# Kernel optimization log

Measured on AMD Instinct MI355X. Metric: run time of the kernel, lower is better.

## Reference

```python
import jax, jax.numpy as jnp
import numpy as np

N = 65536   # base nodes
M = 65536   # union local nodes
E = 1048576 # base edges
EL = 1048576 # local edges
K = 131072  # membership entries
F = 128     # in_channels
H = 128     # hidden_dim
L = 2       # num_layers
OUT = 2
ALPHA = 0.9


def setup_inputs() -> dict:
    key = jax.random.key(0)
    ks = jax.random.split(key, 16)
    s = 1.0 / np.sqrt(H)
    return {
        "x": jax.random.normal(ks[0], (N, F), jnp.float32),
        "edge_index": jax.random.randint(ks[1], (2, E), 0, N, jnp.int64 if jax.config.jax_enable_x64 else jnp.int32),
        "edge_weight": jax.random.uniform(ks[2], (E,), jnp.float32),
        "local_x0": jax.random.normal(ks[3], (M, F), jnp.float32),
        "copy2orig": jax.random.randint(ks[4], (M,), 0, N),
        "local_adj_index": jax.random.randint(ks[5], (2, EL), 0, M),
        "local_adj_value": jax.random.uniform(ks[6], (EL,), jnp.float32),
        "memb_idx": jax.random.randint(ks[7], (K,), 0, M),
        "memb_gid": jax.random.randint(ks[8], (K,), 0, 64),
        "B": 64,
        "Wb_in": jax.random.normal(ks[9], (F, H), jnp.float32) * s,
        "bb_in": jnp.zeros((H,), jnp.float32),
        "Wl_in": jax.random.normal(ks[10], (F, H), jnp.float32) * s,
        "bl_in": jnp.zeros((H,), jnp.float32),
        "W_base": jax.random.normal(ks[11], (L, H, H), jnp.float32) * s,
        "b_base": jnp.zeros((L, H), jnp.float32),
        "W_local": jax.random.normal(ks[12], (L, H, H), jnp.float32) * s,
        "b_local": jnp.zeros((L, H), jnp.float32),
        "Wp": jax.random.normal(ks[13], (H, OUT), jnp.float32) * s,
        "bp": jnp.zeros((OUT,), jnp.float32),
    }


def reference(x, edge_index, edge_weight, local_x0, copy2orig, local_adj_index,
              local_adj_value, memb_idx, memb_gid, B, Wb_in, bb_in, Wl_in, bl_in,
              W_base, b_base, W_local, b_local, Wp, bp):
    n = x.shape[0]
    m = local_x0.shape[0]
    # input projections (dropout is identity in eval mode)
    base_x = jax.nn.relu(x @ Wb_in + bb_in)
    local_x = jax.nn.relu(local_x0 @ Wl_in + bl_in)
    src, dst = edge_index[0], edge_index[1]
    lsrc, ldst = local_adj_index[0], local_adj_index[1]
    for l in range(W_base.shape[0]):
        # base graph propagation: normalized-adjacency spmm then linear+relu
        base_agg = jax.ops.segment_sum(base_x[src] * edge_weight[:, None], dst, num_segments=n)
        base_x = jax.nn.relu(base_agg @ W_base[l] + b_base[l])
        # local union-graph propagation + alpha-mix with base features via copy2orig
        local_agg = jax.ops.segment_sum(local_x[lsrc] * local_adj_value[:, None], ldst, num_segments=m)
        mix = ALPHA * local_agg + (1.0 - ALPHA) * base_x[copy2orig]
        local_x = jax.nn.relu(mix @ W_local[l] + b_local[l])
    # scatter-mean pooling by membership (fused sum + count)
    sub = jax.ops.segment_sum(local_x[memb_idx], memb_gid, num_segments=B)
    cnt = jax.ops.segment_sum(jnp.ones((memb_gid.shape[0], 1), local_x.dtype), memb_gid, num_segments=B)
    sub = sub / jnp.maximum(cnt, 1.0)
    return sub @ Wp + bp
```

## Files before the change

### kernel.cpp

```cpp
#include <hip/hip_runtime.h>

typedef __attribute__((ext_vector_type(8))) short bfrag;
typedef __attribute__((ext_vector_type(4))) float ffrag;

__device__ __forceinline__ ushort f2bf(float f) {
    union { float f; unsigned u; } v{f};
    unsigned r = v.u + 0x7fff + ((v.u >> 16) & 1);
    return (ushort)(r >> 16);
}
__device__ __forceinline__ float bf2f(ushort u) {
    union { unsigned u; float f; } v{(unsigned)u << 16};
    return v.f;
}
__device__ __forceinline__ float bflo(unsigned u) {
    union { unsigned u; float f; } v{u << 16};
    return v.f;
}
__device__ __forceinline__ float bfhi(unsigned u) {
    union { unsigned u; float f; } v{u & 0xffff0000u};
    return v.f;
}

#define WDEC (1.f / 65535.f)


__global__ __launch_bounds__(256) void wprep_zero(const float* __restrict__ Wb_in, const float* __restrict__ Wl_in,
                                                  const float* __restrict__ W_base, const float* __restrict__ W_local,
                                                  ushort* __restrict__ out,
                                                  int* __restrict__ z_a, int* __restrict__ z_b,
                                                  int* __restrict__ z_c, int* __restrict__ z_d) {
    const int bid = blockIdx.x;
    const int t = threadIdx.x;
    if (bid < 384) {
        int idx = bid * 256 + t;
        int mat = idx >> 14;
        int i = idx & 16383;
        int nn = i >> 7, kk = i & 127;
        const float* src;
        switch (mat) {
            case 0: src = Wb_in; break;
            case 1: src = Wl_in; break;
            case 2: src = W_base; break;
            case 3: src = W_base + 16384; break;
            case 4: src = W_local; break;
            default: src = W_local + 16384; break;
        }
        out[(size_t)mat * 16384 + i] = f2bf(src[kk * 128 + nn]);
    } else {
        int i = (bid - 384) * 256 + t;
        if (i < 512) { z_a[i] = 0; z_b[i] = 0; }
        if (i < 64) z_c[i] = 0;
        z_d[i] = 0;
    }
}


#define NB 512
#define BSH 7
#define CH2 2048

__global__ __launch_bounds__(256) void bhist2(const int* __restrict__ b_dst, const int* __restrict__ l_dst,
                                              int* __restrict__ b_cnt, int* __restrict__ l_cnt) {
    __shared__ int h[NB];
    const int t = threadIdx.x;
    h[t] = 0;
    h[t + 256] = 0;
    __syncthreads();
    const int g = blockIdx.x >> 8;
    const int* dst = g ? l_dst : b_dst;
    int* cnt = g ? l_cnt : b_cnt;
    const int base = (blockIdx.x & 255) * 4096;
#pragma unroll
    for (int u = 0; u < 16; ++u)
        atomicAdd(&h[((unsigned)dst[base + u * 256 + t]) >> BSH], 1);
    __syncthreads();
    atomicAdd(&cnt[t], h[t]);
    atomicAdd(&cnt[t + 256], h[t + 256]);
}

__global__ __launch_bounds__(512) void bscan2(const int* __restrict__ b_cnt, int* __restrict__ b_sta, int* __restrict__ b_cur,
                                              const int* __restrict__ l_cnt, int* __restrict__ l_sta, int* __restrict__ l_cur) {
    __shared__ int s[NB];
    const int t = threadIdx.x;
    const int* cnt = blockIdx.x ? l_cnt : b_cnt;
    int* sta = blockIdx.x ? l_sta : b_sta;
    int* cur = blockIdx.x ? l_cur : b_cur;
    int c = cnt[t];
    s[t] = c;
    __syncthreads();
    for (int o = 1; o < NB; o <<= 1) {
        int add = (t >= o) ? s[t - o] : 0;
        __syncthreads();
        s[t] += add;
        __syncthreads();
    }
    sta[t] = s[t] - c;
    cur[t] = s[t] - c;
    if (t == NB - 1) sta[NB] = s[t];
}

__global__ __launch_bounds__(1024) void bucket1b(const int* __restrict__ b_src, const int* __restrict__ b_dst,
                                                 const float* __restrict__ b_w, int* __restrict__ b_cur,
                                                 int2* __restrict__ b_staged,
                                                 const int* __restrict__ l_src, const int* __restrict__ l_dst,
                                                 const float* __restrict__ l_w, int* __restrict__ l_cur,
                                                 int2* __restrict__ l_staged) {
    __shared__ int cnt_s[NB], base_l[NB], base_g[NB], curs[NB];
    __shared__ int2 stage[CH2];
    __shared__ ushort bb[CH2];
    const int t = threadIdx.x;
    const int g = blockIdx.x >> 9;
    const int* src = g ? l_src : b_src;
    const int* dst = g ? l_dst : b_dst;
    const float* w = g ? l_w : b_w;
    int* bcursor = g ? l_cur : b_cur;
    int2* staged = g ? l_staged : b_staged;
    const int base = (blockIdx.x & 511) * CH2;
    if (t < NB) cnt_s[t] = 0;
    __syncthreads();
#pragma unroll
    for (int u = 0; u < CH2 / 1024; ++u) {
        int b = ((unsigned)dst[base + u * 1024 + t]) >> BSH;
        atomicAdd(&cnt_s[b], 1);
    }
    __syncthreads();
    int v = 0;
    if (t < NB) { v = cnt_s[t]; base_l[t] = v; }
    __syncthreads();
    for (int o = 1; o < NB; o <<= 1) {
        int add = 0;
        if (t < NB && t >= o) add = base_l[t - o];
        __syncthreads();
        if (t < NB) base_l[t] += add;
        __syncthreads();
    }
    if (t < NB) {
        int excl = base_l[t] - v;
        base_l[t] = excl;
        curs[t] = excl;
        base_g[t] = atomicAdd(&bcursor[t], v);
    }
    __syncthreads();
#pragma unroll
    for (int u = 0; u < CH2 / 1024; ++u) {
        int e = base + u * 1024 + t;
        int d = dst[e];
        int b = ((unsigned)d) >> BSH;
        int p = atomicAdd(&curs[b], 1);
        stage[p] = make_int2((src[e] & 0xffff) | ((d & 127) << 16), __float_as_int(w[e]));
        bb[p] = (ushort)b;
    }
    __syncthreads();
    for (int i = t; i < CH2; i += 1024) {
        int b = bb[i];
        staged[base_g[b] + (i - base_l[b])] = stage[i];
    }
}

__global__ __launch_bounds__(1024) void bucket2b(const int* __restrict__ b_sta, const int2* __restrict__ b_staged,
                                                 int* __restrict__ b_start, int* __restrict__ b_edges,
                                                 const int* __restrict__ l_sta, const int2* __restrict__ l_staged,
                                                 int* __restrict__ l_start, int* __restrict__ l_edges) {
    __shared__ int cnt[128], excl[128], curs[128];
    const int t = threadIdx.x;
    const int g = blockIdx.x >> 9;
    const int b = blockIdx.x & 511;
    const int* bsta = g ? l_sta : b_sta;
    const int2* staged = g ? l_staged : b_staged;
    int* start = g ? l_start : b_start;
    int* edges = g ? l_edges : b_edges;
    if (t < 128) cnt[t] = 0;
    __syncthreads();
    const int s0 = bsta[b];
    const int s1 = bsta[b + 1];
    for (int i = s0 + t; i < s1; i += 1024) {
        int dl = (staged[i].x >> 16) & 127;
        atomicAdd(&cnt[dl], 1);
    }
    __syncthreads();
    int v = 0;
    if (t < 128) { v = cnt[t]; excl[t] = v; }
    __syncthreads();
    for (int o = 1; o < 128; o <<= 1) {
        int add = 0;
        if (t < 128 && t >= o) add = excl[t - o];
        __syncthreads();
        if (t < 128) excl[t] += add;
        __syncthreads();
    }
    if (t < 128) {
        int e = excl[t] - v;
        curs[t] = e;
        start[b * 128 + t] = s0 + e;
        if (b == 511 && t == 127) start[65536] = s1;
    }
    __syncthreads();
    for (int i = s0 + t; i < s1; i += 1024) {
        int2 se = staged[i];
        int dl = (se.x >> 16) & 127;
        int p = s0 + atomicAdd(&curs[dl], 1);
        float wv = __int_as_float(se.y);
        unsigned wq = (unsigned)(wv * 65535.f + 0.5f);
        edges[p] = (int)(((unsigned)se.x & 0xffffu) | (wq << 16));
    }
}

#define ASTRIDE 136


__global__ __launch_bounds__(256) void gemm_in2(const float* __restrict__ Ab, const float* __restrict__ Al,
                                                const ushort* __restrict__ Wt,
                                                const float* __restrict__ biasb, const float* __restrict__ biasl,
                                                ushort* __restrict__ Yb, ushort* __restrict__ Yl) {
    __shared__ ushort As[64 * ASTRIDE];
    __shared__ ushort Bs[128 * ASTRIDE];
    const int tid = threadIdx.x;
    const int g = blockIdx.x >> 10;
    const float* A = g ? Al : Ab;
    const ushort* W = Wt + (size_t)g * 16384;
    const float* bias = g ? biasl : biasb;
    ushort* Y = g ? Yl : Yb;
    const int r0 = (blockIdx.x & 1023) * 64;

#pragma unroll
    for (int p = 0; p < 8; ++p) {
        int c = p * 256 + tid;
        int row = c >> 5, o4 = (c & 31) * 4;
        float4 v = *(const float4*)(A + (size_t)(r0 + row) * 128 + o4);
        ushort4 u;
        u.x = f2bf(v.x); u.y = f2bf(v.y); u.z = f2bf(v.z); u.w = f2bf(v.w);
        *(ushort4*)&As[row * ASTRIDE + o4] = u;
    }
#pragma unroll
    for (int p = 0; p < 8; ++p) {
        int c = p * 256 + tid;
        int n = c >> 4, o8 = (c & 15) * 8;
        *(uint4*)&Bs[n * ASTRIDE + o8] = *(const uint4*)(W + n * 128 + o8);
    }
    __syncthreads();

    const int lane = tid & 63;
    const int w = tid >> 6;
    const int wm = (w & 1) * 32;
    const int wn = (w >> 1) * 64;
    const int q = lane >> 4;
    const int l16 = lane & 15;

    ffrag acc[2][4];
#pragma unroll
    for (int mt = 0; mt < 2; ++mt)
#pragma unroll
        for (int nt = 0; nt < 4; ++nt) acc[mt][nt] = (ffrag){0.f, 0.f, 0.f, 0.f};

#pragma unroll
    for (int kc = 0; kc < 4; ++kc) {
        bfrag a[2], b[4];
#pragma unroll
        for (int mt = 0; mt < 2; ++mt)
            a[mt] = *(const bfrag*)&As[(wm + mt * 16 + l16) * ASTRIDE + kc * 32 + q * 8];
#pragma unroll
        for (int nt = 0; nt < 4; ++nt)
            b[nt] = *(const bfrag*)&Bs[(wn + nt * 16 + l16) * ASTRIDE + kc * 32 + q * 8];
#pragma unroll
        for (int mt = 0; mt < 2; ++mt)
#pragma unroll
            for (int nt = 0; nt < 4; ++nt)
                acc[mt][nt] = __builtin_amdgcn_mfma_f32_16x16x32_bf16(a[mt], b[nt], acc[mt][nt], 0, 0, 0);
    }

    float bias_v[4];
#pragma unroll
    for (int nt = 0; nt < 4; ++nt) bias_v[nt] = bias[wn + nt * 16 + l16];
#pragma unroll
    for (int mt = 0; mt < 2; ++mt)
#pragma unroll
        for (int nt = 0; nt < 4; ++nt)
#pragma unroll
            for (int r = 0; r < 4; ++r) {
                int row = r0 + wm + mt * 16 + q * 4 + r;
                int col = wn + nt * 16 + l16;
                float v = fmaxf(acc[mt][nt][r] + bias_v[nt], 0.f);
                Y[(size_t)row * 128 + col] = f2bf(v);
            }
}


template <bool MIX>
__global__ __launch_bounds__(256) void gemm_layer(const ushort* __restrict__ A, const ushort* __restrict__ A2,
                                                  const int* __restrict__ ridx,
                                                  const ushort* __restrict__ Wt, const float* __restrict__ bias,
                                                  ushort* __restrict__ Y) {
    __shared__ ushort As[64 * ASTRIDE];
    __shared__ ushort Bs[128 * ASTRIDE];
    const int tid = threadIdx.x;
    const int r0 = blockIdx.x * 64;

#pragma unroll
    for (int p = 0; p < 4; ++p) {
        int c = p * 256 + tid;
        int row = c >> 4, o8 = (c & 15) * 8;
        uint4 v = *(const uint4*)(A + (size_t)(r0 + row) * 128 + o8);
        if (MIX) {
            int rr = ridx[r0 + row];
            uint4 v2 = *(const uint4*)(A2 + (size_t)rr * 128 + o8);
            uint4 o;
            float x0, x1;
            x0 = 0.9f * bflo(v.x) + 0.1f * bflo(v2.x);
            x1 = 0.9f * bfhi(v.x) + 0.1f * bfhi(v2.x);
            o.x = (unsigned)f2bf(x0) | ((unsigned)f2bf(x1) << 16);
            x0 = 0.9f * bflo(v.y) + 0.1f * bflo(v2.y);
            x1 = 0.9f * bfhi(v.y) + 0.1f * bfhi(v2.y);
            o.y = (unsigned)f2bf(x0) | ((unsigned)f2bf(x1) << 16);
            x0 = 0.9f * bflo(v.z) + 0.1f * bflo(v2.z);
            x1 = 0.9f * bfhi(v.z) + 0.1f * bfhi(v2.z);
            o.z = (unsigned)f2bf(x0) | ((unsigned)f2bf(x1) << 16);
            x0 = 0.9f * bflo(v.w) + 0.1f * bflo(v2.w);
            x1 = 0.9f * bfhi(v.w) + 0.1f * bfhi(v2.w);
            o.w = (unsigned)f2bf(x0) | ((unsigned)f2bf(x1) << 16);
            v = o;
        }
        *(uint4*)&As[row * ASTRIDE + o8] = v;
    }
#pragma unroll
    for (int p = 0; p < 8; ++p) {
        int c = p * 256 + tid;
        int n = c >> 4, o8 = (c & 15) * 8;
        *(uint4*)&Bs[n * ASTRIDE + o8] = *(const uint4*)(Wt + n * 128 + o8);
    }
    __syncthreads();

    const int lane = tid & 63;
    const int w = tid >> 6;
    const int wm = (w & 1) * 32;
    const int wn = (w >> 1) * 64;
    const int q = lane >> 4;
    const int l16 = lane & 15;

    ffrag acc[2][4];
#pragma unroll
    for (int mt = 0; mt < 2; ++mt)
#pragma unroll
        for (int nt = 0; nt < 4; ++nt) acc[mt][nt] = (ffrag){0.f, 0.f, 0.f, 0.f};

#pragma unroll
    for (int kc = 0; kc < 4; ++kc) {
        bfrag a[2], b[4];
#pragma unroll
        for (int mt = 0; mt < 2; ++mt)
            a[mt] = *(const bfrag*)&As[(wm + mt * 16 + l16) * ASTRIDE + kc * 32 + q * 8];
#pragma unroll
        for (int nt = 0; nt < 4; ++nt)
            b[nt] = *(const bfrag*)&Bs[(wn + nt * 16 + l16) * ASTRIDE + kc * 32 + q * 8];
#pragma unroll
        for (int mt = 0; mt < 2; ++mt)
#pragma unroll
            for (int nt = 0; nt < 4; ++nt)
                acc[mt][nt] = __builtin_amdgcn_mfma_f32_16x16x32_bf16(a[mt], b[nt], acc[mt][nt], 0, 0, 0);
    }

    float bias_v[4];
#pragma unroll
    for (int nt = 0; nt < 4; ++nt) bias_v[nt] = bias[wn + nt * 16 + l16];
#pragma unroll
    for (int mt = 0; mt < 2; ++mt)
#pragma unroll
        for (int nt = 0; nt < 4; ++nt)
#pragma unroll
            for (int r = 0; r < 4; ++r) {
                int row = r0 + wm + mt * 16 + q * 4 + r;
                int col = wn + nt * 16 + l16;
                float v = fmaxf(acc[mt][nt][r] + bias_v[nt], 0.f);
                Y[(size_t)row * 128 + col] = f2bf(v);
            }
}


__global__ __launch_bounds__(256) void spmm2(const int* __restrict__ bs_start, const int* __restrict__ bs_edges,
                                             const ushort* __restrict__ Xb, ushort* __restrict__ Yb,
                                             const int* __restrict__ ls_start, const int* __restrict__ ls_edges,
                                             const ushort* __restrict__ Xl, ushort* __restrict__ Yl) {
    const int g = blockIdx.x & 1;
    const int* start = g ? ls_start : bs_start;
    const int* edges = g ? ls_edges : bs_edges;
    const ushort* X = g ? Xl : Xb;
    ushort* Y = g ? Yl : Yb;
    int node = (((blockIdx.x >> 1) * 256) + threadIdx.x) >> 5;
    int lane = threadIdx.x & 31;
    int s0 = start[node];
    int s1 = start[node + 1];
    const int f = lane * 4;
    float a0 = 0.f, a1 = 0.f, a2 = 0.f, a3 = 0.f;
    int e = s0;
    for (; e < s1 && (e & 3); ++e) {
        unsigned pe = (unsigned)edges[e];
        float w = (float)(pe >> 16) * WDEC;
        ushort4 v = *(const ushort4*)(X + ((size_t)(pe & 0xffffu) << 7) + f);
        a0 += w * bf2f(v.x); a1 += w * bf2f(v.y); a2 += w * bf2f(v.z); a3 += w * bf2f(v.w);
    }
    for (; e + 8 <= s1; e += 8) {
        int4 pA = *(const int4*)(edges + e);
        int4 pB = *(const int4*)(edges + e + 4);
        ushort4 v0 = *(const ushort4*)(X + ((size_t)((unsigned)pA.x & 0xffffu) << 7) + f);
        ushort4 v1 = *(const ushort4*)(X + ((size_t)((unsigned)pA.y & 0xffffu) << 7) + f);
        ushort4 v2 = *(const ushort4*)(X + ((size_t)((unsigned)pA.z & 0xffffu) << 7) + f);
        ushort4 v3 = *(const ushort4*)(X + ((size_t)((unsigned)pA.w & 0xffffu) << 7) + f);
        ushort4 v4 = *(const ushort4*)(X + ((size_t)((unsigned)pB.x & 0xffffu) << 7) + f);
        ushort4 v5 = *(const ushort4*)(X + ((size_t)((unsigned)pB.y & 0xffffu) << 7) + f);
        ushort4 v6 = *(const ushort4*)(X + ((size_t)((unsigned)pB.z & 0xffffu) << 7) + f);
        ushort4 v7 = *(const ushort4*)(X + ((size_t)((unsigned)pB.w & 0xffffu) << 7) + f);
        float w0 = (float)((unsigned)pA.x >> 16) * WDEC;
        float w1 = (float)((unsigned)pA.y >> 16) * WDEC;
        float w2 = (float)((unsigned)pA.z >> 16) * WDEC;
        float w3 = (float)((unsigned)pA.w >> 16) * WDEC;
        float w4 = (float)((unsigned)pB.x >> 16) * WDEC;
        float w5 = (float)((unsigned)pB.y >> 16) * WDEC;
        float w6 = (float)((unsigned)pB.z >> 16) * WDEC;
        float w7 = (float)((unsigned)pB.w >> 16) * WDEC;
        a0 += w0 * bf2f(v0.x) + w1 * bf2f(v1.x) + w2 * bf2f(v2.x) + w3 * bf2f(v3.x)
            + w4 * bf2f(v4.x) + w5 * bf2f(v5.x) + w6 * bf2f(v6.x) + w7 * bf2f(v7.x);
        a1 += w0 * bf2f(v0.y) + w1 * bf2f(v1.y) + w2 * bf2f(v2.y) + w3 * bf2f(v3.y)
            + w4 * bf2f(v4.y) + w5 * bf2f(v5.y) + w6 * bf2f(v6.y) + w7 * bf2f(v7.y);
        a2 += w0 * bf2f(v0.z) + w1 * bf2f(v1.z) + w2 * bf2f(v2.z) + w3 * bf2f(v3.z)
            + w4 * bf2f(v4.z) + w5 * bf2f(v5.z) + w6 * bf2f(v6.z) + w7 * bf2f(v7.z);
        a3 += w0 * bf2f(v0.w) + w1 * bf2f(v1.w) + w2 * bf2f(v2.w) + w3 * bf2f(v3.w)
            + w4 * bf2f(v4.w) + w5 * bf2f(v5.w) + w6 * bf2f(v6.w) + w7 * bf2f(v7.w);
    }
    for (; e + 4 <= s1; e += 4) {
        int4 pA = *(const int4*)(edges + e);
        ushort4 v0 = *(const ushort4*)(X + ((size_t)((unsigned)pA.x & 0xffffu) << 7) + f);
        ushort4 v1 = *(const ushort4*)(X + ((size_t)((unsigned)pA.y & 0xffffu) << 7) + f);
        ushort4 v2 = *(const ushort4*)(X + ((size_t)((unsigned)pA.z & 0xffffu) << 7) + f);
        ushort4 v3 = *(const ushort4*)(X + ((size_t)((unsigned)pA.w & 0xffffu) << 7) + f);
        float w0 = (float)((unsigned)pA.x >> 16) * WDEC;
        float w1 = (float)((unsigned)pA.y >> 16) * WDEC;
        float w2 = (float)((unsigned)pA.z >> 16) * WDEC;
        float w3 = (float)((unsigned)pA.w >> 16) * WDEC;
        a0 += w0 * bf2f(v0.x) + w1 * bf2f(v1.x) + w2 * bf2f(v2.x) + w3 * bf2f(v3.x);
        a1 += w0 * bf2f(v0.y) + w1 * bf2f(v1.y) + w2 * bf2f(v2.y) + w3 * bf2f(v3.y);
        a2 += w0 * bf2f(v0.z) + w1 * bf2f(v1.z) + w2 * bf2f(v2.z) + w3 * bf2f(v3.z);
        a3 += w0 * bf2f(v0.w) + w1 * bf2f(v1.w) + w2 * bf2f(v2.w) + w3 * bf2f(v3.w);
    }
    for (; e < s1; ++e) {
        unsigned pe = (unsigned)edges[e];
        float w = (float)(pe >> 16) * WDEC;
        ushort4 v = *(const ushort4*)(X + ((size_t)(pe & 0xffffu) << 7) + f);
        a0 += w * bf2f(v.x); a1 += w * bf2f(v.y); a2 += w * bf2f(v.z); a3 += w * bf2f(v.w);
    }
    ushort4 o;
    o.x = f2bf(a0);
    o.y = f2bf(a1);
    o.z = f2bf(a2);
    o.w = f2bf(a3);
    *(ushort4*)(Y + (size_t)node * 128 + f) = o;
}


__global__ __launch_bounds__(256) void pool_hist(const int* __restrict__ memb_gid, int* __restrict__ gcount) {
    __shared__ int h[64];
    int t = threadIdx.x;
    if (t < 64) h[t] = 0;
    __syncthreads();
    int base = blockIdx.x * 1024;
#pragma unroll
    for (int u = 0; u < 4; ++u) atomicAdd(&h[memb_gid[base + u * 256 + t]], 1);
    __syncthreads();
    if (t < 64) atomicAdd(&gcount[t], h[t]);
}

__global__ __launch_bounds__(64) void pool_scan(const int* __restrict__ gcount, int* __restrict__ gstart,
                                                int* __restrict__ cursor) {
    __shared__ int s[64];
    int t = threadIdx.x;
    int c = gcount[t];
    s[t] = c;
    __syncthreads();
    int acc = 0;
    for (int j = 0; j < 64; ++j)
        if (j < t) acc += s[j];
    gstart[t] = acc;
    cursor[t] = acc;
    if (t == 63) gstart[64] = acc + c;
}

__global__ __launch_bounds__(256) void pool_scatter(const int* __restrict__ memb_idx,
                                                    const int* __restrict__ memb_gid,
                                                    int* __restrict__ cursor, int* __restrict__ sorted_idx) {
    __shared__ int lhist[64];
    __shared__ int lbase[64];
    __shared__ int loff[1024];
    int t = threadIdx.x;
    if (t < 64) lhist[t] = 0;
    __syncthreads();
    int base = blockIdx.x * 1024;
    int g[4], ix[4];
#pragma unroll
    for (int u = 0; u < 4; ++u) {
        int e = base + u * 256 + t;
        g[u] = memb_gid[e];
        ix[u] = memb_idx[e];
        loff[u * 256 + t] = atomicAdd(&lhist[g[u]], 1);
    }
    __syncthreads();
    if (t < 64) lbase[t] = atomicAdd(&cursor[t], lhist[t]);
    __syncthreads();
#pragma unroll
    for (int u = 0; u < 4; ++u) {
        int pos = lbase[g[u]] + loff[u * 256 + t];
        sorted_idx[pos] = ix[u];
    }
}

__global__ __launch_bounds__(256) void pool_accum(const int* __restrict__ gstart, const int* __restrict__ sorted_idx,
                                                  const ushort* __restrict__ X, float* __restrict__ gsum) {
    const int g = blockIdx.x >> 5;
    const int sgm = blockIdx.x & 31;
    const int gs = gstart[g];
    const int cnt = gstart[g + 1] - gs;
    const int e_begin = gs + ((cnt * sgm) >> 5);
    const int e_end = gs + ((cnt * (sgm + 1)) >> 5);
    const int t = threadIdx.x;
    const int fp = t & 63;
    const int sub = t >> 6;
    float ax = 0.f, ay = 0.f;
#pragma unroll 4
    for (int e = e_begin + sub; e < e_end; e += 4) {
        int idx = sorted_idx[e];
        ushort2 u = *(const ushort2*)(X + (size_t)idx * 128 + fp * 2);
        ax += bf2f(u.x);
        ay += bf2f(u.y);
    }
    __shared__ float sx[256], sy[256];
    sx[t] = ax;
    sy[t] = ay;
    __syncthreads();
    if (t < 64) {
        atomicAdd(&gsum[g * 128 + fp * 2 + 0], sx[t] + sx[t + 64] + sx[t + 128] + sx[t + 192]);
        atomicAdd(&gsum[g * 128 + fp * 2 + 1], sy[t] + sy[t + 64] + sy[t + 128] + sy[t + 192]);
    }
}


__global__ __launch_bounds__(128) void final_kernel(const float* __restrict__ gsum, const int* __restrict__ gcnt,
                                                    const float* __restrict__ Wp, const float* __restrict__ bp,
                                                    float* __restrict__ out) {
    int t = threadIdx.x;
    int g = t >> 1;
    int o = t & 1;
    float inv = 1.f / fmaxf((float)gcnt[g], 1.f);
    float acc = bp[o];
    for (int f = 0; f < 128; ++f) acc += gsum[g * 128 + f] * inv * Wp[f * 2 + o];
    out[g * 2 + o] = acc;
}


extern "C" void kernel_launch(void* const* d_in, const int* in_sizes, int n_in,
                              void* d_out, int out_size, void* d_ws, size_t ws_size,
                              hipStream_t stream) {
    const float* x              = (const float*)d_in[0];
    const int*   edge_index     = (const int*)d_in[1];
    const float* edge_weight    = (const float*)d_in[2];
    const float* local_x0       = (const float*)d_in[3];
    const int*   copy2orig      = (const int*)d_in[4];
    const int*   local_adj_idx  = (const int*)d_in[5];
    const float* local_adj_val  = (const float*)d_in[6];
    const int*   memb_idx       = (const int*)d_in[7];
    const int*   memb_gid       = (const int*)d_in[8];
    const float* Wb_in          = (const float*)d_in[10];
    const float* bb_in          = (const float*)d_in[11];
    const float* Wl_in          = (const float*)d_in[12];
    const float* bl_in          = (const float*)d_in[13];
    const float* W_base         = (const float*)d_in[14];
    const float* b_base         = (const float*)d_in[15];
    const float* W_local        = (const float*)d_in[16];
    const float* b_local        = (const float*)d_in[17];
    const float* Wp             = (const float*)d_in[18];
    const float* bp             = (const float*)d_in[19];
    float* out = (float*)d_out;

    constexpr int N = 65536, M = 65536, E = 1048576, EL = 1048576, K = 131072, H = 128;

    char* wsb = (char*)d_ws;
    size_t off = 0;
    auto alloc = [&](size_t bytes) -> char* {
        char* p = wsb + off;
        off += (bytes + 255) & ~(size_t)255;
        return p;
    };
    int*    bs_start = (int*)alloc((size_t)(N + 1) * 4);
    int*    bs_edges = (int*)alloc((size_t)E * 4);
    int2*   bs_stage = (int2*)alloc((size_t)E * 8);
    int*    bs_bcnt  = (int*)alloc(NB * 4);
    int*    bs_bsta  = (int*)alloc((NB + 1) * 4);
    int*    bs_bcur  = (int*)alloc(NB * 4);
    int*    ls_start = (int*)alloc((size_t)(M + 1) * 4);
    int*    ls_edges = (int*)alloc((size_t)EL * 4);
    int2*   ls_stage = (int2*)alloc((size_t)EL * 8);
    int*    ls_bcnt  = (int*)alloc(NB * 4);
    int*    ls_bsta  = (int*)alloc((NB + 1) * 4);
    int*    ls_bcur  = (int*)alloc(NB * 4);
    ushort* bufA     = (ushort*)alloc((size_t)N * H * 2);
    ushort* bufB     = (ushort*)alloc((size_t)M * H * 2);
    ushort* bufC     = (ushort*)alloc((size_t)N * H * 2);
    ushort* bufD     = (ushort*)alloc((size_t)M * H * 2);
    ushort* wt       = (ushort*)alloc((size_t)6 * 16384 * 2);
    int*    p_gcnt   = (int*)alloc(64 * 4);
    int*    p_gstart = (int*)alloc(65 * 4);
    int*    p_cursor = (int*)alloc(64 * 4);
    int*    p_sorted = (int*)alloc((size_t)K * 4);
    float*  pool_sum = (float*)alloc(64 * 128 * 4);

    const int* b_src = edge_index;
    const int* b_dst = edge_index + E;
    const int* l_src = local_adj_idx;
    const int* l_dst = local_adj_idx + EL;

    wprep_zero<<<416, 256, 0, stream>>>(Wb_in, Wl_in, W_base, W_local, wt,
                                        bs_bcnt, ls_bcnt, p_gcnt, (int*)pool_sum);

    bhist2<<<512, 256, 0, stream>>>(b_dst, l_dst, bs_bcnt, ls_bcnt);
    bscan2<<<2, 512, 0, stream>>>(bs_bcnt, bs_bsta, bs_bcur, ls_bcnt, ls_bsta, ls_bcur);
    bucket1b<<<1024, 1024, 0, stream>>>(b_src, b_dst, edge_weight, bs_bcur, bs_stage,
                                        l_src, l_dst, local_adj_val, ls_bcur, ls_stage);
    bucket2b<<<1024, 1024, 0, stream>>>(bs_bsta, bs_stage, bs_start, bs_edges,
                                        ls_bsta, ls_stage, ls_start, ls_edges);

    pool_hist<<<K / 1024, 256, 0, stream>>>(memb_gid, p_gcnt);
    pool_scan<<<1, 64, 0, stream>>>(p_gcnt, p_gstart, p_cursor);
    pool_scatter<<<K / 1024, 256, 0, stream>>>(memb_idx, memb_gid, p_cursor, p_sorted);

    gemm_in2<<<2048, 256, 0, stream>>>(x, local_x0, wt, bb_in, bl_in, bufA, bufB);

    for (int l = 0; l < 2; ++l) {
        spmm2<<<16384, 256, 0, stream>>>(bs_start, bs_edges, bufA, bufC,
                                         ls_start, ls_edges, bufB, bufD);
        gemm_layer<false><<<N / 64, 256, 0, stream>>>(bufC, nullptr, nullptr,
                                                      wt + (size_t)(2 + l) * 16384, b_base + (size_t)l * H, bufA);
        gemm_layer<true><<<M / 64, 256, 0, stream>>>(bufD, bufA, copy2orig,
                                                     wt + (size_t)(4 + l) * 16384, b_local + (size_t)l * H, bufB);
    }

    pool_accum<<<64 * 32, 256, 0, stream>>>(p_gstart, p_sorted, bufB, pool_sum);
    final_kernel<<<1, 128, 0, stream>>>(pool_sum, p_gcnt, Wp, bp, out);
}
```

Before: 424.6 us.

## Build CSR with direct per-node atomics and split SpMM feature halves

Replaces the two-level bucket sort (bucket histogram, staged bucket scatter, per-bucket local sort) with a direct CSR build: per-node global atomic histogram, a three-pass prefix scan, and atomic-cursor scatter of packed edges. This removes the staging buffer and one full pass over the edges, at the cost of heavy global atomic contention and non-deterministic edge order within each row. The SpMM also splits each node's 128 features across two blocks, each lane gathering 2 bf16 values instead of 4. That doubles the grid for more parallelism but rereads the edge lists twice and narrows the gather loads.

```diff
diff --git a/kernel.cpp b/kernel.cpp
--- a/kernel.cpp
+++ b/kernel.cpp
@@ -27,8 +27,8 @@
 __global__ __launch_bounds__(256) void wprep_zero(const float* __restrict__ Wb_in, const float* __restrict__ Wl_in,
                                                   const float* __restrict__ W_base, const float* __restrict__ W_local,
                                                   ushort* __restrict__ out,
-                                                  int* __restrict__ z_a, int* __restrict__ z_b,
-                                                  int* __restrict__ z_c, int* __restrict__ z_d) {
+                                                  int* __restrict__ b_cnt, int* __restrict__ l_cnt,
+                                                  int* __restrict__ gcnt, int* __restrict__ psum) {
     const int bid = blockIdx.x;
     const int t = threadIdx.x;
     if (bid < 384) {
@@ -48,160 +48,104 @@
         out[(size_t)mat * 16384 + i] = f2bf(src[kk * 128 + nn]);
     } else {
         int i = (bid - 384) * 256 + t;
-        if (i < 512) { z_a[i] = 0; z_b[i] = 0; }
-        if (i < 64) z_c[i] = 0;
-        z_d[i] = 0;
-    }
-}
-
-
-#define NB 512
-#define BSH 7
-#define CH2 2048
-
-__global__ __launch_bounds__(256) void bhist2(const int* __restrict__ b_dst, const int* __restrict__ l_dst,
-                                              int* __restrict__ b_cnt, int* __restrict__ l_cnt) {
-    __shared__ int h[NB];
-    const int t = threadIdx.x;
-    h[t] = 0;
-    h[t + 256] = 0;
-    __syncthreads();
-    const int g = blockIdx.x >> 8;
+        if (i < 65536) b_cnt[i] = 0;
+        else if (i < 131072) l_cnt[i - 65536] = 0;
+        else if (i < 131136) gcnt[i - 131072] = 0;
+        else if (i < 139328) psum[i - 131136] = 0;
+    }
+}
+
+
+__global__ __launch_bounds__(256) void csr_hist(const int* __restrict__ b_dst, const int* __restrict__ l_dst,
+                                                int* __restrict__ b_cnt, int* __restrict__ l_cnt) {
+    const int g = blockIdx.x >> 10;
     const int* dst = g ? l_dst : b_dst;
     int* cnt = g ? l_cnt : b_cnt;
-    const int base = (blockIdx.x & 255) * 4096;
-#pragma unroll
-    for (int u = 0; u < 16; ++u)
-        atomicAdd(&h[((unsigned)dst[base + u * 256 + t]) >> BSH], 1);
-    __syncthreads();
-    atomicAdd(&cnt[t], h[t]);
-    atomicAdd(&cnt[t + 256], h[t + 256]);
-}
-
-__global__ __launch_bounds__(512) void bscan2(const int* __restrict__ b_cnt, int* __restrict__ b_sta, int* __restrict__ b_cur,
-                                              const int* __restrict__ l_cnt, int* __restrict__ l_sta, int* __restrict__ l_cur) {
-    __shared__ int s[NB];
+    const int base = (blockIdx.x & 1023) * 1024 + threadIdx.x;
+#pragma unroll
+    for (int u = 0; u < 4; ++u)
+        atomicAdd(&cnt[dst[base + u * 256]], 1);
+}
+
+__global__ __launch_bounds__(256) void csr_scan1(const int* __restrict__ b_cnt, const int* __restrict__ l_cnt,
+                                                 int* __restrict__ b_start, int* __restrict__ l_start,
+                                                 int* __restrict__ bsum) {
+    __shared__ int sh[256];
     const int t = threadIdx.x;
-    const int* cnt = blockIdx.x ? l_cnt : b_cnt;
-    int* sta = blockIdx.x ? l_sta : b_sta;
-    int* cur = blockIdx.x ? l_cur : b_cur;
-    int c = cnt[t];
-    s[t] = c;
-    __syncthreads();
-    for (int o = 1; o < NB; o <<= 1) {
-        int add = (t >= o) ? s[t - o] : 0;
+    const int g = blockIdx.x >> 6;
+    const int blk = blockIdx.x & 63;
+    const int* cnt = g ? l_cnt : b_cnt;
+    int* out = g ? l_start : b_start;
+    int4 v = ((const int4*)cnt)[blk * 256 + t];
+    int s = v.x + v.y + v.z + v.w;
+    sh[t] = s;
+    __syncthreads();
+    for (int o = 1; o < 256; o <<= 1) {
+        int add = (t >= o) ? sh[t - o] : 0;
         __syncthreads();
-        s[t] += add;
+        sh[t] += add;
         __syncthreads();
     }
-    sta[t] = s[t] - c;
-    cur[t] = s[t] - c;
-    if (t == NB - 1) sta[NB] = s[t];
-}
-
-__global__ __launch_bounds__(1024) void bucket1b(const int* __restrict__ b_src, const int* __restrict__ b_dst,
-                                                 const float* __restrict__ b_w, int* __restrict__ b_cur,
-                                                 int2* __restrict__ b_staged,
-                                                 const int* __restrict__ l_src, const int* __restrict__ l_dst,
-                                                 const float* __restrict__ l_w, int* __restrict__ l_cur,
-                                                 int2* __restrict__ l_staged) {
-    __shared__ int cnt_s[NB], base_l[NB], base_g[NB], curs[NB];
-    __shared__ int2 stage[CH2];
-    __shared__ ushort bb[CH2];
+    int excl = sh[t] - s;
+    int4 o4;
+    o4.x = excl;
+    o4.y = excl + v.x;
+    o4.z = excl + v.x + v.y;
+    o4.w = excl + v.x + v.y + v.z;
+    ((int4*)out)[blk * 256 + t] = o4;
+    if (t == 255) bsum[blockIdx.x] = sh[255];
+}
+
+__global__ __launch_bounds__(128) void csr_scan2(const int* __restrict__ bsum, int* __restrict__ bbase,
+                                                 int* __restrict__ b_start, int* __restrict__ l_start) {
+    __shared__ int s[128];
     const int t = threadIdx.x;
-    const int g = blockIdx.x >> 9;
+    s[t] = bsum[t];
+    __syncthreads();
+    const int sb = t & 64;
+    int acc = 0;
+    for (int j = sb; j < t; ++j) acc += s[j];
+    bbase[t] = acc;
+    if (t == 63) b_start[65536] = acc + s[63];
+    if (t == 127) l_start[65536] = acc + s[127];
+}
+
+__global__ __launch_bounds__(256) void csr_scan3(const int* __restrict__ bbase,
+                                                 int* __restrict__ b_start, int* __restrict__ b_cur,
+                                                 int* __restrict__ l_start, int* __restrict__ l_cur) {
+    const int t = threadIdx.x;
+    const int g = blockIdx.x >> 6;
+    const int blk = blockIdx.x & 63;
+    const int off = bbase[blockIdx.x];
+    int* out = g ? l_start : b_start;
+    int* cur = g ? l_cur : b_cur;
+    int4 v = ((const int4*)out)[blk * 256 + t];
+    v.x += off; v.y += off; v.z += off; v.w += off;
+    ((int4*)out)[blk * 256 + t] = v;
+    ((int4*)cur)[blk * 256 + t] = v;
+}
+
+__global__ __launch_bounds__(256) void csr_scatter(const int* __restrict__ b_src, const int* __restrict__ b_dst,
+                                                   const float* __restrict__ b_w, int* __restrict__ b_cur,
+                                                   int* __restrict__ b_edges,
+                                                   const int* __restrict__ l_src, const int* __restrict__ l_dst,
+                                                   const float* __restrict__ l_w, int* __restrict__ l_cur,
+                                                   int* __restrict__ l_edges) {
+    const int g = blockIdx.x >> 10;
     const int* src = g ? l_src : b_src;
     const int* dst = g ? l_dst : b_dst;
     const float* w = g ? l_w : b_w;
-    int* bcursor = g ? l_cur : b_cur;
-    int2* staged = g ? l_staged : b_staged;
-    const int base = (blockIdx.x & 511) * CH2;
-    if (t < NB) cnt_s[t] = 0;
-    __syncthreads();
-#pragma unroll
-    for (int u = 0; u < CH2 / 1024; ++u) {
-        int b = ((unsigned)dst[base + u * 1024 + t]) >> BSH;
-        atomicAdd(&cnt_s[b], 1);
-    }
-    __syncthreads();
-    int v = 0;
-    if (t < NB) { v = cnt_s[t]; base_l[t] = v; }
-    __syncthreads();
-    for (int o = 1; o < NB; o <<= 1) {
-        int add = 0;
-        if (t < NB && t >= o) add = base_l[t - o];
-        __syncthreads();
-        if (t < NB) base_l[t] += add;
-        __syncthreads();
-    }
-    if (t < NB) {
-        int excl = base_l[t] - v;
-        base_l[t] = excl;
-        curs[t] = excl;
-        base_g[t] = atomicAdd(&bcursor[t], v);
-    }
-    __syncthreads();
-#pragma unroll
-    for (int u = 0; u < CH2 / 1024; ++u) {
-        int e = base + u * 1024 + t;
+    int* cur = g ? l_cur : b_cur;
+    int* edges = g ? l_edges : b_edges;
+    const int base = (blockIdx.x & 1023) * 1024 + threadIdx.x;
+#pragma unroll
+    for (int u = 0; u < 4; ++u) {
+        int e = base + u * 256;
         int d = dst[e];
-        int b = ((unsigned)d) >> BSH;
-        int p = atomicAdd(&curs[b], 1);
-        stage[p] = make_int2((src[e] & 0xffff) | ((d & 127) << 16), __float_as_int(w[e]));
-        bb[p] = (ushort)b;
-    }
-    __syncthreads();
-    for (int i = t; i < CH2; i += 1024) {
-        int b = bb[i];
-        staged[base_g[b] + (i - base_l[b])] = stage[i];
-    }
-}
-
-__global__ __launch_bounds__(1024) void bucket2b(const int* __restrict__ b_sta, const int2* __restrict__ b_staged,
-                                                 int* __restrict__ b_start, int* __restrict__ b_edges,
-                                                 const int* __restrict__ l_sta, const int2* __restrict__ l_staged,
-                                                 int* __restrict__ l_start, int* __restrict__ l_edges) {
-    __shared__ int cnt[128], excl[128], curs[128];
-    const int t = threadIdx.x;
-    const int g = blockIdx.x >> 9;
-    const int b = blockIdx.x & 511;
-    const int* bsta = g ? l_sta : b_sta;
-    const int2* staged = g ? l_staged : b_staged;
-    int* start = g ? l_start : b_start;
-    int* edges = g ? l_edges : b_edges;
-    if (t < 128) cnt[t] = 0;
-    __syncthreads();
-    const int s0 = bsta[b];
-    const int s1 = bsta[b + 1];
-    for (int i = s0 + t; i < s1; i += 1024) {
-        int dl = (staged[i].x >> 16) & 127;
-        atomicAdd(&cnt[dl], 1);
-    }
-    __syncthreads();
-    int v = 0;
-    if (t < 128) { v = cnt[t]; excl[t] = v; }
-    __syncthreads();
-    for (int o = 1; o < 128; o <<= 1) {
-        int add = 0;
-        if (t < 128 && t >= o) add = excl[t - o];
-        __syncthreads();
-        if (t < 128) excl[t] += add;
-        __syncthreads();
-    }
-    if (t < 128) {
-        int e = excl[t] - v;
-        curs[t] = e;
-        start[b * 128 + t] = s0 + e;
-        if (b == 511 && t == 127) start[65536] = s1;
-    }
-    __syncthreads();
-    for (int i = s0 + t; i < s1; i += 1024) {
-        int2 se = staged[i];
-        int dl = (se.x >> 16) & 127;
-        int p = s0 + atomicAdd(&curs[dl], 1);
-        float wv = __int_as_float(se.y);
-        unsigned wq = (unsigned)(wv * 65535.f + 0.5f);
-        edges[p] = (int)(((unsigned)se.x & 0xffffu) | (wq << 16));
+        unsigned wq = (unsigned)(w[e] * 65535.f + 0.5f);
+        int packed = (int)(((unsigned)src[e] & 0xffffu) | (wq << 16));
+        int pos = atomicAdd(&cur[d], 1);
+        edges[pos] = packed;
     }
 }
 
@@ -380,34 +324,36 @@
                                              const int* __restrict__ ls_start, const int* __restrict__ ls_edges,
                                              const ushort* __restrict__ Xl, ushort* __restrict__ Yl) {
     const int g = blockIdx.x & 1;
+    const int h = (blockIdx.x >> 1) & 1;
     const int* start = g ? ls_start : bs_start;
     const int* edges = g ? ls_edges : bs_edges;
     const ushort* X = g ? Xl : Xb;
     ushort* Y = g ? Yl : Yb;
-    int node = (((blockIdx.x >> 1) * 256) + threadIdx.x) >> 5;
-    int lane = threadIdx.x & 31;
-    int s0 = start[node];
-    int s1 = start[node + 1];
-    const int f = lane * 4;
-    float a0 = 0.f, a1 = 0.f, a2 = 0.f, a3 = 0.f;
+    const int node = ((blockIdx.x >> 2) * 256 + threadIdx.x) >> 5;
+    const int lane = threadIdx.x & 31;
+    const int fo = h * 64 + lane * 2;
+    const int s0 = start[node];
+    const int s1 = start[node + 1];
+    float a0 = 0.f, a1 = 0.f;
     int e = s0;
     for (; e < s1 && (e & 3); ++e) {
         unsigned pe = (unsigned)edges[e];
         float w = (float)(pe >> 16) * WDEC;
-        ushort4 v = *(const ushort4*)(X + ((size_t)(pe & 0xffffu) << 7) + f);
-        a0 += w * bf2f(v.x); a1 += w * bf2f(v.y); a2 += w * bf2f(v.z); a3 += w * bf2f(v.w);
+        ushort2 v = *(const ushort2*)(X + ((size_t)(pe & 0xffffu) << 7) + fo);
+        a0 += w * bf2f(v.x);
+        a1 += w * bf2f(v.y);
     }
     for (; e + 8 <= s1; e += 8) {
         int4 pA = *(const int4*)(edges + e);
         int4 pB = *(const int4*)(edges + e + 4);
-        ushort4 v0 = *(const ushort4*)(X + ((size_t)((unsigned)pA.x & 0xffffu) << 7) + f);
-        ushort4 v1 = *(const ushort4*)(X + ((size_t)((unsigned)pA.y & 0xffffu) << 7) + f);
-        ushort4 v2 = *(const ushort4*)(X + ((size_t)((unsigned)pA.z & 0xffffu) << 7) + f);
-        ushort4 v3 = *(const ushort4*)(X + ((size_t)((unsigned)pA.w & 0xffffu) << 7) + f);
-        ushort4 v4 = *(const ushort4*)(X + ((size_t)((unsigned)pB.x & 0xffffu) << 7) + f);
-        ushort4 v5 = *(const ushort4*)(X + ((size_t)((unsigned)pB.y & 0xffffu) << 7) + f);
-        ushort4 v6 = *(const ushort4*)(X + ((size_t)((unsigned)pB.z & 0xffffu) << 7) + f);
-        ushort4 v7 = *(const ushort4*)(X + ((size_t)((unsigned)pB.w & 0xffffu) << 7) + f);
+        ushort2 v0 = *(const ushort2*)(X + ((size_t)((unsigned)pA.x & 0xffffu) << 7) + fo);
+        ushort2 v1 = *(const ushort2*)(X + ((size_t)((unsigned)pA.y & 0xffffu) << 7) + fo);
+        ushort2 v2 = *(const ushort2*)(X + ((size_t)((unsigned)pA.z & 0xffffu) << 7) + fo);
+        ushort2 v3 = *(const ushort2*)(X + ((size_t)((unsigned)pA.w & 0xffffu) << 7) + fo);
+        ushort2 v4 = *(const ushort2*)(X + ((size_t)((unsigned)pB.x & 0xffffu) << 7) + fo);
+        ushort2 v5 = *(const ushort2*)(X + ((size_t)((unsigned)pB.y & 0xffffu) << 7) + fo);
+        ushort2 v6 = *(const ushort2*)(X + ((size_t)((unsigned)pB.z & 0xffffu) << 7) + fo);
+        ushort2 v7 = *(const ushort2*)(X + ((size_t)((unsigned)pB.w & 0xffffu) << 7) + fo);
         float w0 = (float)((unsigned)pA.x >> 16) * WDEC;
         float w1 = (float)((unsigned)pA.y >> 16) * WDEC;
         float w2 = (float)((unsigned)pA.z >> 16) * WDEC;
@@ -420,38 +366,31 @@
             + w4 * bf2f(v4.x) + w5 * bf2f(v5.x) + w6 * bf2f(v6.x) + w7 * bf2f(v7.x);
         a1 += w0 * bf2f(v0.y) + w1 * bf2f(v1.y) + w2 * bf2f(v2.y) + w3 * bf2f(v3.y)
             + w4 * bf2f(v4.y) + w5 * bf2f(v5.y) + w6 * bf2f(v6.y) + w7 * bf2f(v7.y);
-        a2 += w0 * bf2f(v0.z) + w1 * bf2f(v1.z) + w2 * bf2f(v2.z) + w3 * bf2f(v3.z)
-            + w4 * bf2f(v4.z) + w5 * bf2f(v5.z) + w6 * bf2f(v6.z) + w7 * bf2f(v7.z);
-        a3 += w0 * bf2f(v0.w) + w1 * bf2f(v1.w) + w2 * bf2f(v2.w) + w3 * bf2f(v3.w)
-            + w4 * bf2f(v4.w) + w5 * bf2f(v5.w) + w6 * bf2f(v6.w) + w7 * bf2f(v7.w);
     }
     for (; e + 4 <= s1; e += 4) {
         int4 pA = *(const int4*)(edges + e);
-        ushort4 v0 = *(const ushort4*)(X + ((size_t)((unsigned)pA.x & 0xffffu) << 7) + f);
-        ushort4 v1 = *(const ushort4*)(X + ((size_t)((unsigned)pA.y & 0xffffu) << 7) + f);
-        ushort4 v2 = *(const ushort4*)(X + ((size_t)((unsigned)pA.z & 0xffffu) << 7) + f);
-        ushort4 v3 = *(const ushort4*)(X + ((size_t)((unsigned)pA.w & 0xffffu) << 7) + f);
+        ushort2 v0 = *(const ushort2*)(X + ((size_t)((unsigned)pA.x & 0xffffu) << 7) + fo);
+        ushort2 v1 = *(const ushort2*)(X + ((size_t)((unsigned)pA.y & 0xffffu) << 7) + fo);
+        ushort2 v2 = *(const ushort2*)(X + ((size_t)((unsigned)pA.z & 0xffffu) << 7) + fo);
+        ushort2 v3 = *(const ushort2*)(X + ((size_t)((unsigned)pA.w & 0xffffu) << 7) + fo);
         float w0 = (float)((unsigned)pA.x >> 16) * WDEC;
         float w1 = (float)((unsigned)pA.y >> 16) * WDEC;
         float w2 = (float)((unsigned)pA.z >> 16) * WDEC;
         float w3 = (float)((unsigned)pA.w >> 16) * WDEC;
         a0 += w0 * bf2f(v0.x) + w1 * bf2f(v1.x) + w2 * bf2f(v2.x) + w3 * bf2f(v3.x);
         a1 += w0 * bf2f(v0.y) + w1 * bf2f(v1.y) + w2 * bf2f(v2.y) + w3 * bf2f(v3.y);
-        a2 += w0 * bf2f(v0.z) + w1 * bf2f(v1.z) + w2 * bf2f(v2.z) + w3 * bf2f(v3.z);
-        a3 += w0 * bf2f(v0.w) + w1 * bf2f(v1.w) + w2 * bf2f(v2.w) + w3 * bf2f(v3.w);
     }
     for (; e < s1; ++e) {
         unsigned pe = (unsigned)edges[e];
         float w = (float)(pe >> 16) * WDEC;
-        ushort4 v = *(const ushort4*)(X + ((size_t)(pe & 0xffffu) << 7) + f);
-        a0 += w * bf2f(v.x); a1 += w * bf2f(v.y); a2 += w * bf2f(v.z); a3 += w * bf2f(v.w);
-    }
-    ushort4 o;
+        ushort2 v = *(const ushort2*)(X + ((size_t)(pe & 0xffffu) << 7) + fo);
+        a0 += w * bf2f(v.x);
+        a1 += w * bf2f(v.y);
+    }
+    ushort2 o;
     o.x = f2bf(a0);
     o.y = f2bf(a1);
-    o.z = f2bf(a2);
-    o.w = f2bf(a3);
-    *(ushort4*)(Y + (size_t)node * 128 + f) = o;
+    *(ushort2*)(Y + (size_t)node * 128 + fo) = o;
 }
 
 
@@ -588,16 +527,14 @@
     };
     int*    bs_start = (int*)alloc((size_t)(N + 1) * 4);
     int*    bs_edges = (int*)alloc((size_t)E * 4);
-    int2*   bs_stage = (int2*)alloc((size_t)E * 8);
-    int*    bs_bcnt  = (int*)alloc(NB * 4);
-    int*    bs_bsta  = (int*)alloc((NB + 1) * 4);
-    int*    bs_bcur  = (int*)alloc(NB * 4);
+    int*    bs_cnt   = (int*)alloc((size_t)N * 4);
+    int*    bs_cur   = (int*)alloc((size_t)N * 4);
     int*    ls_start = (int*)alloc((size_t)(M + 1) * 4);
     int*    ls_edges = (int*)alloc((size_t)EL * 4);
-    int2*   ls_stage = (int2*)alloc((size_t)EL * 8);
-    int*    ls_bcnt  = (int*)alloc(NB * 4);
-    int*    ls_bsta  = (int*)alloc((NB + 1) * 4);
-    int*    ls_bcur  = (int*)alloc(NB * 4);
+    int*    ls_cnt   = (int*)alloc((size_t)M * 4);
+    int*    ls_cur   = (int*)alloc((size_t)M * 4);
+    int*    sc_bsum  = (int*)alloc(128 * 4);
+    int*    sc_bbase = (int*)alloc(128 * 4);
     ushort* bufA     = (ushort*)alloc((size_t)N * H * 2);
     ushort* bufB     = (ushort*)alloc((size_t)M * H * 2);
     ushort* bufC     = (ushort*)alloc((size_t)N * H * 2);
@@ -614,15 +551,15 @@
     const int* l_src = local_adj_idx;
     const int* l_dst = local_adj_idx + EL;
 
-    wprep_zero<<<416, 256, 0, stream>>>(Wb_in, Wl_in, W_base, W_local, wt,
-                                        bs_bcnt, ls_bcnt, p_gcnt, (int*)pool_sum);
-
-    bhist2<<<512, 256, 0, stream>>>(b_dst, l_dst, bs_bcnt, ls_bcnt);
-    bscan2<<<2, 512, 0, stream>>>(bs_bcnt, bs_bsta, bs_bcur, ls_bcnt, ls_bsta, ls_bcur);
-    bucket1b<<<1024, 1024, 0, stream>>>(b_src, b_dst, edge_weight, bs_bcur, bs_stage,
-                                        l_src, l_dst, local_adj_val, ls_bcur, ls_stage);
-    bucket2b<<<1024, 1024, 0, stream>>>(bs_bsta, bs_stage, bs_start, bs_edges,
-                                        ls_bsta, ls_stage, ls_start, ls_edges);
+    wprep_zero<<<929, 256, 0, stream>>>(Wb_in, Wl_in, W_base, W_local, wt,
+                                        bs_cnt, ls_cnt, p_gcnt, (int*)pool_sum);
+
+    csr_hist<<<2048, 256, 0, stream>>>(b_dst, l_dst, bs_cnt, ls_cnt);
+    csr_scan1<<<128, 256, 0, stream>>>(bs_cnt, ls_cnt, bs_start, ls_start, sc_bsum);
+    csr_scan2<<<1, 128, 0, stream>>>(sc_bsum, sc_bbase, bs_start, ls_start);
+    csr_scan3<<<128, 256, 0, stream>>>(sc_bbase, bs_start, bs_cur, ls_start, ls_cur);
+    csr_scatter<<<2048, 256, 0, stream>>>(b_src, b_dst, edge_weight, bs_cur, bs_edges,
+                                          l_src, l_dst, local_adj_val, ls_cur, ls_edges);
 
     pool_hist<<<K / 1024, 256, 0, stream>>>(memb_gid, p_gcnt);
     pool_scan<<<1, 64, 0, stream>>>(p_gcnt, p_gstart, p_cursor);
@@ -631,7 +568,7 @@
     gemm_in2<<<2048, 256, 0, stream>>>(x, local_x0, wt, bb_in, bl_in, bufA, bufB);
 
     for (int l = 0; l < 2; ++l) {
-        spmm2<<<16384, 256, 0, stream>>>(bs_start, bs_edges, bufA, bufC,
+        spmm2<<<32768, 256, 0, stream>>>(bs_start, bs_edges, bufA, bufC,
                                          ls_start, ls_edges, bufB, bufD);
         gemm_layer<false><<<N / 64, 256, 0, stream>>>(bufC, nullptr, nullptr,
                                                       wt + (size_t)(2 + l) * 16384, b_base + (size_t)l * H, bufA);
```

Result: slower. 661.0 us (+55.7%).
